# Kernel optimization log

Measured on AMD Instinct MI355X. Metric: run time of the kernel, lower is better.

## Reference

```python
import jax, jax.numpy as jnp
import numpy as np

N = 32       # number of variables (per-var LSTMs)
L = 128      # window length
D = 128      # hidden dim
HEADS = 8
TAU_MAX = 5
ALPHA = 0.7  # attn_decay_alpha
B = 128      # number of time-ordered windows


def setup_inputs() -> dict:
    key = jax.random.key(0)
    ks = jax.random.split(key, 20)
    s = 0.1
    f = lambda k, shape: (jax.random.normal(k, shape, jnp.float32) * s)
    return {
        "X": jax.random.normal(ks[0], (B, L, N), jnp.float32),
        # per-variable encoder LSTM (input size 1): W_ih (N,4D), W_hh (N,4D,D), combined-style biases kept separate
        "enc_Wih": f(ks[1], (N, 4 * D)),
        "enc_Whh": f(ks[2], (N, 4 * D, D)),
        "enc_b": f(ks[3], (N, 4 * D)),            # b_ih + b_hh merged (mathematically identical)
        "pool_w": f(ks[4], (N, D)),
        "pool_b": f(ks[5], (N,)),
        # shared MultiheadAttention params (torch layout: in_proj (3D,D))
        "in_proj_w": f(ks[6], (3 * D, D)),
        "in_proj_b": f(ks[7], (3 * D,)),
        "out_proj_w": f(ks[8], (D, D)),
        "out_proj_b": f(ks[9], (D,)),
        # per-variable decoder: init_h/init_c Linear(d,d), LSTM(1,d) (input is all-zeros so W_ih drops out), out Linear(d,1)
        "dec_initH_w": f(ks[10], (N, D, D)),
        "dec_initH_b": f(ks[11], (N, D)),
        "dec_initC_w": f(ks[12], (N, D, D)),
        "dec_initC_b": f(ks[13], (N, D)),
        "dec_Whh": f(ks[14], (N, 4 * D, D)),
        "dec_bih": f(ks[15], (N, 4 * D)),
        "dec_bhh": f(ks[16], (N, 4 * D)),
        "dec_out_w": f(ks[17], (N, D)),
        "dec_out_b": f(ks[18], (N,)),
    }


def _lstm_cell(gates, c):
    # torch gate order: i, f, g, o
    i, fg, g, o = jnp.split(gates, 4, axis=-1)
    i = jax.nn.sigmoid(i); fg = jax.nn.sigmoid(fg)
    g = jnp.tanh(g); o = jax.nn.sigmoid(o)
    c = fg * c + i * g
    h = o * jnp.tanh(c)
    return h, c


def _encode(X, Wih, Whh, b, pool_w, pool_b):
    # X: (B,L,N); encoder consumes first L-1 steps of each variable, batched over all N vars
    x = jnp.transpose(X[:, :-1, :], (1, 2, 0))  # (T, N, B)
    Bn = X.shape[0]
    h0 = jnp.zeros((N, Bn, D), X.dtype)

    def step(carry, x_t):  # x_t: (N,B)
        h, c = carry
        gates = (x_t[..., None] * Wih[:, None, :]
                 + jnp.einsum('nbd,ngd->nbg', h, Whh)
                 + b[:, None, :])
        h, c = _lstm_cell(gates, c)
        return (h, c), h

    _, H = jax.lax.scan(step, (h0, h0), x)  # H: (T,N,B,D)
    # TemporalAttnPool: softmax over time of a linear score, weighted sum
    scores = jnp.einsum('tnbd,nd->tnb', H, pool_w) + pool_b[None, :, None]
    a = jax.nn.softmax(scores, axis=0)
    C = jnp.einsum('tnb,tnbd->bnd', a, H)  # (B,N,D)
    return C


def _mha(Q, KV, in_w, in_b, out_w, out_b):
    dh = D // HEADS
    q = Q @ in_w[:D].T + in_b[:D]
    k = KV @ in_w[D:2 * D].T + in_b[D:2 * D]
    v = KV @ in_w[2 * D:].T + in_b[2 * D:]
    sp = lambda x: x.reshape(x.shape[0], x.shape[1], HEADS, dh)
    q, k, v = sp(q), sp(k), sp(v)
    scores = jnp.einsum('bqhd,bkhd->bhqk', q, k) / float(np.sqrt(dh))
    attn = jax.nn.softmax(scores, axis=-1)
    o = jnp.einsum('bhqk,bkhd->bqhd', attn, v).reshape(Q.shape)
    return o @ out_w.T + out_b


def _cross_attend(C, in_w, in_b, out_w, out_b):
    Bn = C.shape[0]
    tmax = min(TAU_MAX, Bn - 1)
    if tmax <= 0:
        return C
    out_sum = jnp.zeros_like(C)
    w_sum = jnp.zeros((Bn, 1, 1), C.dtype)
    for tau in range(1, tmax + 1):  # small fixed loop over lags
        o = _mha(C[tau:], C[:-tau], in_w, in_b, out_w, out_b)
        w = float(np.exp(-ALPHA * (tau - 1)))  # attn_agg == 'decay'
        out_sum = out_sum.at[tau:].add(o * w)
        w_sum = w_sum.at[tau:].add(w)
    out = out_sum / jnp.clip(w_sum, 1e-8)
    return C + out  # residual=True


def _decode(C_star, iHw, iHb, iCw, iCb, Whh, bih, bhh, ow, ob):
    # h0/c0 from tanh(Linear(c_star)); LSTM input is all-zeros so input term reduces to b_ih
    h0 = jnp.tanh(jnp.einsum('bnd,ned->nbe', C_star, iHw) + iHb[:, None, :])
    c0 = jnp.tanh(jnp.einsum('bnd,ned->nbe', C_star, iCw) + iCb[:, None, :])
    b = (bih + bhh)[:, None, :]  # (N,1,4D)

    def step(carry, _):
        h, c = carry
        gates = jnp.einsum('nbd,ngd->nbg', h, Whh) + b
        h, c = _lstm_cell(gates, c)
        o = jnp.einsum('nbd,nd->nb', h, ow) + ob[:, None]
        return (h, c), o

    _, O = jax.lax.scan(step, (h0, c0), None, length=L)  # (L,N,B)
    recon = jnp.transpose(O[:L - 1], (2, 0, 1))  # (B,L-1,N)
    pred = O[L - 1].T                            # (B,N)
    return recon, pred


def reference(X, enc_Wih, enc_Whh, enc_b, pool_w, pool_b,
              in_proj_w, in_proj_b, out_proj_w, out_proj_b,
              dec_initH_w, dec_initH_b, dec_initC_w, dec_initC_b,
              dec_Whh, dec_bih, dec_bhh, dec_out_w, dec_out_b):
    C = _encode(X, enc_Wih, enc_Whh, enc_b, pool_w, pool_b)
    C_star = _cross_attend(C, in_proj_w, in_proj_b, out_proj_w, out_proj_b)
    recon, pred = _decode(C_star, dec_initH_w, dec_initH_b, dec_initC_w, dec_initC_b,
                          dec_Whh, dec_bih, dec_bhh, dec_out_w, dec_out_b)
    return recon, pred, C_star
```

## Files before the change

kernel.cpp:

```cpp
#include <hip/hip_runtime.h>
#include <hip/hip_bf16.h>

typedef unsigned short ushort_t;
typedef unsigned int uint_t;

#define DD   128
#define G4   512
#define BT   16
#define NB   128
#define NV   32

#define OFF_WIH   0
#define OFF_EB    16384
#define OFF_PW    32768
#define OFF_PB    36864
#define OFF_INW   37120
#define OFF_INB   86272
#define OFF_OUTW  86784
#define OFF_OUTB  103168
#define OFF_IHB   103424
#define OFF_ICB   107520
#define OFF_DBIH  111616
#define OFF_DBHH  128000
#define OFF_DOW   144384
#define OFF_DOB   148480
#define P_TOTAL   148736
#define OFF_FLAGS (OFF_PB + 32)

typedef __attribute__((ext_vector_type(8))) short bf16x8;
typedef __attribute__((ext_vector_type(4))) float f32x4;

__device__ __forceinline__ float bf2f(ushort_t u) {
    union { uint_t i; float f; } x; x.i = ((uint_t)u) << 16; return x.f;
}
__device__ __forceinline__ ushort_t f2bf(float f) {
    __hip_bfloat16 h = __float2bfloat16(f);
    return *(ushort_t*)&h;
}
__device__ __forceinline__ uint_t f2u(float f) {
    union { float f; uint_t i; } x; x.f = f; return x.i;
}
__device__ __forceinline__ float u2f(uint_t u) {
    union { uint_t i; float f; } x; x.i = u; return x.f;
}
__device__ __forceinline__ float exp2_f(float x) {
    float r; asm("v_exp_f32 %0, %1" : "=v"(r) : "v"(x)); return r;
}
__device__ __forceinline__ float sigmoid_f(float x) {
    return __builtin_amdgcn_rcpf(1.f + exp2_f(x * -1.442695041f));
}
__device__ __forceinline__ float tanh_f(float x) {
    return 1.f - 2.f * __builtin_amdgcn_rcpf(exp2_f(x * 2.885390082f) + 1.f);
}
__device__ __forceinline__ uint_t cvt_pk_bf16(float a, float b) {
    uint_t r; asm("v_cvt_pk_bf16_f32 %0, %1, %2" : "=v"(r) : "v"(a), "v"(b)); return r;
}
__device__ __forceinline__ bf16x8 pack8(f32x4 a, f32x4 b) {
    union { uint_t u[4]; bf16x8 v; } x;
    x.u[0] = cvt_pk_bf16(a.x, a.y); x.u[1] = cvt_pk_bf16(a.z, a.w);
    x.u[2] = cvt_pk_bf16(b.x, b.y); x.u[3] = cvt_pk_bf16(b.z, b.w);
    return x.v;
}
__device__ __forceinline__ float swz_bcast_l15(float v) {
    return u2f((uint_t)__builtin_amdgcn_ds_swizzle((int)f2u(v), 0x000F));
}
__device__ __forceinline__ void store_out(void* out, long idx, float v, int bf) {
    if (bf) ((ushort_t*)out)[idx] = f2bf(v);
    else    ((float*)out)[idx]    = v;
}
#define LBAR() do { asm volatile("s_waitcnt lgkmcnt(0)" ::: "memory"); \
                    __builtin_amdgcn_s_barrier(); } while (0)

__device__ __forceinline__ int wave_probe(const void* p, int elems) {
    int cap = elems < 1024 ? elems : 1024;
    int lane = threadIdx.x & 63;
    const ushort_t* u = (const ushort_t*)p;
    int cnt = 0, tot = 0;
    for (int j = lane; j < cap; j += 64) {
        ushort_t x = u[j];
        float af = fabsf(bf2f(x));
        tot++;
        if (x == 0 || (af > 1e-7f && af < 100.f)) cnt++;
    }
    #pragma unroll
    for (int off = 32; off >= 1; off >>= 1) {
        cnt += __shfl_xor(cnt, off);
        tot += __shfl_xor(tot, off);
    }
    return (cnt * 10 >= tot * 9) ? 1 : 0;
}

struct Ptr19 { const void* p[19]; };

__global__ __launch_bounds__(256) void prep_kernel(Ptr19 a, float* __restrict__ P,
                                                   float* __restrict__ Xc) {
    __shared__ float tile[32][65];
    if (blockIdx.x < 581) {
        int base = blockIdx.x * 256;
        int src, o0, size;
        if      (base < OFF_EB)   { src = 1;  o0 = base - OFF_WIH;  size = 16384; }
        else if (base < OFF_PW)   { src = 3;  o0 = base - OFF_EB;   size = 16384; }
        else if (base < OFF_PB)   { src = 4;  o0 = base - OFF_PW;   size = 4096;  }
        else if (base < OFF_INW)  { src = 5;  o0 = base - OFF_PB;   size = 32;    }
        else if (base < OFF_INB)  { src = 6;  o0 = base - OFF_INW;  size = 49152; }
        else if (base < OFF_OUTW) { src = 7;  o0 = base - OFF_INB;  size = 384;   }
        else if (base < OFF_OUTB) { src = 8;  o0 = base - OFF_OUTW; size = 16384; }
        else if (base < OFF_IHB)  { src = 9;  o0 = base - OFF_OUTB; size = 128;   }
        else if (base < OFF_ICB)  { src = 11; o0 = base - OFF_IHB;  size = 4096;  }
        else if (base < OFF_DBIH) { src = 13; o0 = base - OFF_ICB;  size = 4096;  }
        else if (base < OFF_DBHH) { src = 15; o0 = base - OFF_DBIH; size = 16384; }
        else if (base < OFF_DOW)  { src = 16; o0 = base - OFF_DBHH; size = 16384; }
        else if (base < OFF_DOB)  { src = 17; o0 = base - OFF_DOW;  size = 4096;  }
        else                      { src = 18; o0 = base - OFF_DOB;  size = 32;    }
        int bf = wave_probe(a.p[src], size);
        int off = o0 + (int)threadIdx.x;
        if (off < size)
            P[base + threadIdx.x] = bf ? bf2f(((const ushort_t*)a.p[src])[off])
                                       : ((const float*)a.p[src])[off];
    } else if (blockIdx.x < 837) {
        int bf = wave_probe(a.p[0], 1024);
        int idx2 = blockIdx.x - 581;
        int bt = (idx2 & 3) * 32, tn0 = (idx2 >> 2) * 64;
        const void* src = a.p[0];
        int tx = threadIdx.x & 63, ty = threadIdx.x >> 6;
        #pragma unroll
        for (int k = 0; k < 8; k++) {
            int row = ty * 8 + k;
            int idx = (bt + row) * 4096 + tn0 + tx;
            tile[row][tx] = bf ? bf2f(((const ushort_t*)src)[idx]) : ((const float*)src)[idx];
        }
        __syncthreads();
        int bx = threadIdx.x & 31, tyy = threadIdx.x >> 5;
        #pragma unroll
        for (int k = 0; k < 8; k++) {
            int tn = tn0 + tyy * 8 + k;
            int t = tn >> 5, nn = tn & 31;
            Xc[t * 4096 + nn * 128 + bt + bx] = tile[bx][tyy * 8 + k];
        }
    } else {
        int which = blockIdx.x - 837;
        int src = (which == 0) ? 0 : (which == 1) ? 2 : (which == 2) ? 10
                : (which == 3) ? 12 : 14;
        int flag = wave_probe(a.p[src], 1024);
        if (threadIdx.x == 0) P[OFF_FLAGS + which] = (float)flag;
    }
}

__global__ __launch_bounds__(512, 2) void enc_kernel(
    const float* __restrict__ Xc, const void* __restrict__ Wraw,
    const float* __restrict__ P, float* __restrict__ Cout)
{
    const int n = blockIdx.y, b0 = blockIdx.x * BT;
    const int tid = threadIdx.x;
    const int w = tid >> 6, lane = tid & 63;
    const int l15 = lane & 15, quad = lane >> 4;
    const int wbf = P[OFF_FLAGS + 1] > 0.5f;
    const int bown = b0 + l15;

    __shared__ alignas(16) ushort_t hS[2][16 * 136];
    for (int i = tid; i < 16 * 136; i += 512) hS[0][i] = 0;

    bf16x8 afrag[4][4];
    #pragma unroll
    for (int typ = 0; typ < 4; typ++) {
        const int g = typ * 128 + 16 * w + l15;
        #pragma unroll
        for (int kc = 0; kc < 4; kc++) {
            const int base = (n * G4 + g) * DD + 32 * kc + 8 * quad;
            if (wbf) {
                afrag[typ][kc] = *(const bf16x8*)((const ushort_t*)Wraw + base);
            } else {
                const float* fp = (const float*)Wraw + base;
                afrag[typ][kc] = pack8(*(const f32x4*)fp, *(const f32x4*)(fp + 4));
            }
        }
    }

    bf16x8 pfrag[4];
    #pragma unroll
    for (int kc = 0; kc < 4; kc++) {
        bf16x8 tmp;
        #pragma unroll
        for (int j = 0; j < 8; j++)
            tmp[j] = (l15 == 0 || l15 == 8)
                   ? (short)f2bf(P[OFF_PW + n * DD + 32 * kc + 8 * quad + j]) : (short)0;
        pfrag[kc] = tmp;
    }

    f32x4 bias4[4], wih4[4];
    #pragma unroll
    for (int typ = 0; typ < 4; typ++) {
        int base = n * G4 + typ * 128 + 16 * w + 4 * quad;
        bias4[typ] = *(const f32x4*)&P[OFF_EB + base];
        wih4[typ]  = *(const f32x4*)&P[OFF_WIH + base];
    }
    const float pb_r = P[OFF_PB + n];
    const f32x4 pb4 = {pb_r, pb_r, pb_r, pb_r};

    float cst[4] = {0.f, 0.f, 0.f, 0.f};
    f32x4 hpair[2];
    hpair[0] = f32x4{0.f, 0.f, 0.f, 0.f};
    hpair[1] = f32x4{0.f, 0.f, 0.f, 0.f};
    f32x4 Cacc   = {0.f, 0.f, 0.f, 0.f};
    float lR = 0.f, pend = 0.f;

    const float* xnext = Xc + n * 128 + bown;
    float xq = *xnext;
    xnext += 4096;

    if (w & 4) __builtin_amdgcn_s_setprio(1);

#define ENC_STEP(T, RB)                                                              \
    do {                                                                             \
        LBAR();                                                                      \
        bf16x8 bh[4];                                                                \
        _Pragma("unroll")                                                            \
        for (int kc = 0; kc < 4; kc++)                                               \
            bh[kc] = *(const bf16x8*)&hS[RB][l15 * 136 + 32 * kc + 8 * quad];        \
        if ((T) >= 2) {         \
            float e = __expf(pend);                                                  \
            lR += e;                                                                 \
            f32x4 ev = {e, e, e, e};                                                 \
            Cacc += ev * hpair[RB];                                                  \
        }                                                                            \
        f32x4 xv = {xq, xq, xq, xq};                                                 \
        f32x4 acc[4];                                                                \
        _Pragma("unroll")                                                            \
        for (int typ = 0; typ < 4; typ++)                                            \
            acc[typ] = __builtin_amdgcn_mfma_f32_16x16x32_bf16(                      \
                afrag[typ][0], bh[0], bias4[typ] + xv * wih4[typ], 0, 0, 0);         \
        f32x4 accP = __builtin_amdgcn_mfma_f32_16x16x32_bf16(pfrag[0], bh[0], pb4, 0, 0, 0); \
        xq = *xnext; xnext += 4096;    \
        _Pragma("unroll")                                                            \
        for (int kc = 1; kc < 4; kc++) {                                             \
            accP = __builtin_amdgcn_mfma_f32_16x16x32_bf16(pfrag[kc], bh[kc], accP, 0, 0, 0); \
            _Pragma("unroll")                                                        \
            for (int typ = 0; typ < 4; typ++)                                        \
                acc[typ] = __builtin_amdgcn_mfma_f32_16x16x32_bf16(afrag[typ][kc], bh[kc], acc[typ], 0, 0, 0); \
        }                                                                            \
        if ((T) >= 1) pend = swz_bcast_l15(accP[0]);   \
        float hh[4];                                                                 \
        _Pragma("unroll")                                                            \
        for (int r = 0; r < 4; r++) {                                                \
            float ii = sigmoid_f(acc[0][r]);                                         \
            float ff = sigmoid_f(acc[1][r]);                                         \
            float g2 = tanh_f(acc[2][r]);                                            \
            float oo = sigmoid_f(acc[3][r]);                                         \
            float cc = ff * cst[r] + ii * g2;                                        \
            cst[r] = cc;                                                             \
            hh[r] = oo * tanh_f(cc);                                                 \
        }                                                                            \
        hpair[RB].x = hh[0]; hpair[RB].y = hh[1];                                    \
        hpair[RB].z = hh[2]; hpair[RB].w = hh[3];                                    \
        uint2 hw;                                                                    \
        hw.x = cvt_pk_bf16(hh[0], hh[1]);                                            \
        hw.y = cvt_pk_bf16(hh[2], hh[3]);                                            \
        *(uint2*)&hS[(RB) ^ 1][l15 * 136 + 16 * w + 4 * quad] = hw;                  \
    } while (0)

    for (int tp = 0; tp < 63; tp++) {
        ENC_STEP(2 * tp, 0);
        ENC_STEP(2 * tp + 1, 1);
    }
    ENC_STEP(126, 0);
#undef ENC_STEP

    LBAR();
    {
        float e = __expf(pend);
        lR += e;
        f32x4 ev = {e, e, e, e};
        Cacc += ev * hpair[1];

        f32x4 accP = __builtin_amdgcn_mfma_f32_16x16x32_bf16(
            pfrag[0], *(const bf16x8*)&hS[1][l15 * 136 + 8 * quad], pb4, 0, 0, 0);
        #pragma unroll
        for (int kc = 1; kc < 4; kc++) {
            bf16x8 bh = *(const bf16x8*)&hS[1][l15 * 136 + 32 * kc + 8 * quad];
            accP = __builtin_amdgcn_mfma_f32_16x16x32_bf16(pfrag[kc], bh, accP, 0, 0, 0);
        }
        float e2 = __expf(swz_bcast_l15(accP[0]));
        lR += e2;
        f32x4 ev2 = {e2, e2, e2, e2};
        Cacc += ev2 * hpair[0];
    }
    float inv = 1.f / lR;
    f32x4 iv = {inv, inv, inv, inv};
    f32x4 cv = Cacc * iv;
    *(f32x4*)&Cout[bown * (NV * DD) + n * DD + 16 * w + 4 * quad] = cv;
}

__global__ __launch_bounds__(256) void qkv_kernel(
    const float* __restrict__ C, const float* __restrict__ P,
    float* __restrict__ q, float* __restrict__ k, float* __restrict__ v)
{
    int b = blockIdx.x, p = blockIdx.y, tid = threadIdx.x;
    int j = tid & 127, half = tid >> 7;
    __shared__ float Cb[NV * DD];
    for (int i = tid; i < NV * DD; i += 256) Cb[i] = C[b * (NV * DD) + i];
    __syncthreads();

    const float* wrow = P + OFF_INW + (p * DD + j) * DD;
    float bias = P[OFF_INB + p * DD + j];
    float acc[16];
    #pragma unroll
    for (int nn = 0; nn < 16; nn++) acc[nn] = bias;

    for (int dc = 0; dc < DD; dc += 8) {
        float4 w0 = *(const float4*)&wrow[dc];
        float4 w1 = *(const float4*)&wrow[dc + 4];
        #pragma unroll
        for (int nn = 0; nn < 16; nn++) {
            const float* cb = &Cb[(half * 16 + nn) * DD + dc];
            float4 c0 = *(float4*)&cb[0];
            float4 c1 = *(float4*)&cb[4];
            acc[nn] += c0.x * w0.x + c0.y * w0.y + c0.z * w0.z + c0.w * w0.w
                     + c1.x * w1.x + c1.y * w1.y + c1.z * w1.z + c1.w * w1.w;
        }
    }
    float* dst = (p == 0) ? q : (p == 1) ? k : v;
    for (int nn = 0; nn < 16; nn++)
        dst[b * (NV * DD) + (half * 16 + nn) * DD + j] = acc[nn];
}

__global__ __launch_bounds__(128) void attn_kernel(
    const float* __restrict__ q, const float* __restrict__ k, const float* __restrict__ v,
    const float* __restrict__ C, const float* __restrict__ P,
    float* __restrict__ Cstar, void* __restrict__ dout)
{
    int b = blockIdx.x, half = blockIdx.y, tid = threadIdx.x;
    int obf = P[OFF_FLAGS + 0] > 0.5f;
    int n0 = half * 16;
    __shared__ float Qs[16 * DD], Ks[NV * DD], Vs[NV * DD];
    float* Os = Ks;
    for (int i = tid; i < 16 * DD; i += 128) Qs[i] = q[b * (NV * DD) + n0 * DD + i];
    __syncthreads();

    int hh = tid >> 4, qi = tid & 15;
    float qreg[16];
    #pragma unroll
    for (int u = 0; u < 4; u++) {
        float4 t4 = *(float4*)&Qs[qi * DD + hh * 16 + 4 * u];
        qreg[4*u] = t4.x; qreg[4*u+1] = t4.y; qreg[4*u+2] = t4.z; qreg[4*u+3] = t4.w;
    }

    float Oacc[16];
    #pragma unroll
    for (int u = 0; u < 16; u++) Oacc[u] = 0.f;
    float wsum = 0.f;
    int tmax = (b < 5) ? b : 5;

    float4 kr[8], vr[8];
#define ATT_LOAD(TAU)                                                            \
    do {                                                                         \
        const float4* kp = (const float4*)&k[(b - (TAU)) * (NV * DD)];           \
        const float4* vp = (const float4*)&v[(b - (TAU)) * (NV * DD)];           \
        _Pragma("unroll")                                                        \
        for (int u = 0; u < 8; u++) {                                            \
            kr[u] = kp[tid + 128 * u];                                           \
            vr[u] = vp[tid + 128 * u];                                           \
        }                                                                        \
    } while (0)

    if (tmax >= 1) ATT_LOAD(1);

    for (int tau = 1; tau <= tmax; tau++) {
        __syncthreads();
        #pragma unroll
        for (int u = 0; u < 8; u++) {
            ((float4*)Ks)[tid + 128 * u] = kr[u];
            ((float4*)Vs)[tid + 128 * u] = vr[u];
        }
        __syncthreads();
        if (tau < tmax) ATT_LOAD(tau + 1);

        float s[NV];
        #pragma unroll
        for (int kk = 0; kk < NV; kk++) {
            float a = 0.f;
            #pragma unroll
            for (int u = 0; u < 4; u++) {
                float4 kv = *(float4*)&Ks[kk * DD + hh * 16 + 4 * u];
                a += qreg[4*u] * kv.x + qreg[4*u+1] * kv.y
                   + qreg[4*u+2] * kv.z + qreg[4*u+3] * kv.w;
            }
            s[kk] = a * 0.25f;
        }
        float mm = s[0];
        #pragma unroll
        for (int kk = 1; kk < NV; kk++) mm = fmaxf(mm, s[kk]);
        float ssum = 0.f;
        #pragma unroll
        for (int kk = 0; kk < NV; kk++) { s[kk] = __expf(s[kk] - mm); ssum += s[kk]; }
        float wdk = __expf(-0.7f * (float)(tau - 1));
        wsum += wdk;
        float wr = wdk / ssum;
        #pragma unroll
        for (int u = 0; u < 4; u++) {
            float ax = 0.f, ay = 0.f, az = 0.f, aw = 0.f;
            #pragma unroll
            for (int kk = 0; kk < NV; kk++) {
                float4 vv = *(float4*)&Vs[kk * DD + hh * 16 + 4 * u];
                ax += s[kk] * vv.x; ay += s[kk] * vv.y;
                az += s[kk] * vv.z; aw += s[kk] * vv.w;
            }
            Oacc[4*u] += wr * ax; Oacc[4*u+1] += wr * ay;
            Oacc[4*u+2] += wr * az; Oacc[4*u+3] += wr * aw;
        }
    }
#undef ATT_LOAD

    __syncthreads();
    float winv = (b > 0) ? 1.f / wsum : 0.f;
    #pragma unroll
    for (int u = 0; u < 16; u++)
        Os[qi * DD + hh * 16 + u] = Oacc[u] * winv;
    __syncthreads();

    int j = tid;
    const float* wrow = P + OFF_OUTW + j * DD;
    float obias = P[OFF_OUTB + j];
    for (int nn = 0; nn < 16; nn++) {
        float a = (b > 0) ? obias : 0.f;
        for (int dc = 0; dc < DD; dc += 8) {
            float4 w0 = *(const float4*)&wrow[dc];
            float4 w1 = *(const float4*)&wrow[dc + 4];
            float4 o0 = *(float4*)&Os[nn * DD + dc];
            float4 o1 = *(float4*)&Os[nn * DD + dc + 4];
            a += o0.x*w0.x + o0.y*w0.y + o0.z*w0.z + o0.w*w0.w
               + o1.x*w1.x + o1.y*w1.y + o1.z*w1.z + o1.w*w1.w;
        }
        int nng = n0 + nn;
        float cs = C[b * (NV * DD) + nng * DD + j] + a;
        Cstar[b * (NV * DD) + nng * DD + j] = cs;
        store_out(dout, 524288 + b * (NV * DD) + nng * DD + j, cs, obf);
    }
}

__global__ __launch_bounds__(512, 2) void dec_kernel(
    const float* __restrict__ Cstar,
    const void* __restrict__ iHw, const void* __restrict__ iCw,
    const void* __restrict__ Wraw,
    const float* __restrict__ P, void* __restrict__ out)
{
    const int n = blockIdx.y, b0 = blockIdx.x * BT;
    const int tid = threadIdx.x;
    const int w = tid >> 6, lane = tid & 63;
    const int l15 = lane & 15, quad = lane >> 4;
    const int obf = P[OFF_FLAGS + 0] > 0.5f;
    const int hbf = P[OFF_FLAGS + 2] > 0.5f;
    const int cbf = P[OFF_FLAGS + 3] > 0.5f;
    const int wbf = P[OFF_FLAGS + 4] > 0.5f;
    const int bown = b0 + l15;

    __shared__ alignas(16) ushort_t hS[2][16 * 136];

    bf16x8 cstB[4];
    #pragma unroll
    for (int kc = 0; kc < 4; kc++) {
        const float* cp = &Cstar[bown * (NV * DD) + n * DD + 32 * kc + 8 * quad];
        cstB[kc] = pack8(*(const f32x4*)&cp[0], *(const f32x4*)&cp[4]);
    }
    float cst[4];
    {
        f32x4 hAcc = *(const f32x4*)&P[OFF_IHB + n * DD + 16 * w + 4 * quad];
        f32x4 cAcc = *(const f32x4*)&P[OFF_ICB + n * DD + 16 * w + 4 * quad];
        #pragma unroll
        for (int kc = 0; kc < 4; kc++) {
            const int base = (n * DD + 16 * w + l15) * DD + 32 * kc + 8 * quad;
            bf16x8 wA;
            if (hbf) wA = *(const bf16x8*)((const ushort_t*)iHw + base);
            else {
                const float* fp = (const float*)iHw + base;
                wA = pack8(*(const f32x4*)fp, *(const f32x4*)(fp + 4));
            }
            hAcc = __builtin_amdgcn_mfma_f32_16x16x32_bf16(wA, cstB[kc], hAcc, 0, 0, 0);
            if (cbf) wA = *(const bf16x8*)((const ushort_t*)iCw + base);
            else {
                const float* fp = (const float*)iCw + base;
                wA = pack8(*(const f32x4*)fp, *(const f32x4*)(fp + 4));
            }
            cAcc = __builtin_amdgcn_mfma_f32_16x16x32_bf16(wA, cstB[kc], cAcc, 0, 0, 0);
        }
        float h0 = tanh_f(hAcc[0]), h1 = tanh_f(hAcc[1]);
        float h2 = tanh_f(hAcc[2]), h3 = tanh_f(hAcc[3]);
        #pragma unroll
        for (int r = 0; r < 4; r++) cst[r] = tanh_f(cAcc[r]);
        uint2 hw;
        hw.x = cvt_pk_bf16(h0, h1);
        hw.y = cvt_pk_bf16(h2, h3);
        *(uint2*)&hS[0][l15 * 136 + 16 * w + 4 * quad] = hw;
    }

    bf16x8 afrag[4][4];
    #pragma unroll
    for (int typ = 0; typ < 4; typ++) {
        const int g = typ * 128 + 16 * w + l15;
        #pragma unroll
        for (int kc = 0; kc < 4; kc++) {
            const int base = (n * G4 + g) * DD + 32 * kc + 8 * quad;
            if (wbf) {
                afrag[typ][kc] = *(const bf16x8*)((const ushort_t*)Wraw + base);
            } else {
                const float* fp = (const float*)Wraw + base;
                afrag[typ][kc] = pack8(*(const f32x4*)fp, *(const f32x4*)(fp + 4));
            }
        }
    }

    bf16x8 pfrag[4];
    #pragma unroll
    for (int kc = 0; kc < 4; kc++) {
        bf16x8 tmp;
        #pragma unroll
        for (int j = 0; j < 8; j++)
            tmp[j] = (l15 == 0) ? (short)f2bf(P[OFF_DOW + n * DD + 32 * kc + 8 * quad + j]) : (short)0;
        pfrag[kc] = tmp;
    }

    f32x4 bias4[4];
    #pragma unroll
    for (int typ = 0; typ < 4; typ++) {
        int base = n * G4 + typ * 128 + 16 * w + 4 * quad;
        f32x4 b1 = *(const f32x4*)&P[OFF_DBIH + base];
        f32x4 b2 = *(const f32x4*)&P[OFF_DBHH + base];
        bias4[typ] = b1 + b2;
    }
    const float ob_r = P[OFF_DOB + n];
    const f32x4 ob4 = {ob_r, ob_r, ob_r, ob_r};

    if (w & 4) __builtin_amdgcn_s_setprio(1);

#define DEC_STEP(T, RB)                                                              \
    do {                                                                             \
        LBAR();                                                                      \
        bf16x8 bh[4];                                                                \
        _Pragma("unroll")                                                            \
        for (int kc = 0; kc < 4; kc++)                                               \
            bh[kc] = *(const bf16x8*)&hS[RB][l15 * 136 + 32 * kc + 8 * quad];        \
        f32x4 acc[4];                                                                \
        _Pragma("unroll")                                                            \
        for (int typ = 0; typ < 4; typ++)                                            \
            acc[typ] = __builtin_amdgcn_mfma_f32_16x16x32_bf16(afrag[typ][0], bh[0], bias4[typ], 0, 0, 0); \
        _Pragma("unroll")                                                            \
        for (int kc = 1; kc < 4; kc++)                                               \
            _Pragma("unroll")                                                        \
            for (int typ = 0; typ < 4; typ++)                                        \
                acc[typ] = __builtin_amdgcn_mfma_f32_16x16x32_bf16(afrag[typ][kc], bh[kc], acc[typ], 0, 0, 0); \
        if (w == ((T) & 7)) {    \
            f32x4 accP = __builtin_amdgcn_mfma_f32_16x16x32_bf16(pfrag[0], bh[0], ob4, 0, 0, 0); \
            _Pragma("unroll")                                                        \
            for (int kc = 1; kc < 4; kc++)                                           \
                accP = __builtin_amdgcn_mfma_f32_16x16x32_bf16(pfrag[kc], bh[kc], accP, 0, 0, 0); \
            if ((T) > 0 && quad == 0)                                                \
                store_out(out, (long)bown * 4064 + (long)((T) - 1) * NV + n, accP[0], obf); \
        }                                                                            \
        float hh[4];                                                                 \
        _Pragma("unroll")                                                            \
        for (int r = 0; r < 4; r++) {                                                \
            float ii = sigmoid_f(acc[0][r]);                                         \
            float ff = sigmoid_f(acc[1][r]);                                         \
            float g2 = tanh_f(acc[2][r]);                                            \
            float oo = sigmoid_f(acc[3][r]);                                         \
            float cc = ff * cst[r] + ii * g2;                                        \
            cst[r] = cc;                                                             \
            hh[r] = oo * tanh_f(cc);                                                 \
        }                                                                            \
        uint2 hw;                                                                    \
        hw.x = cvt_pk_bf16(hh[0], hh[1]);                                            \
        hw.y = cvt_pk_bf16(hh[2], hh[3]);                                            \
        *(uint2*)&hS[(RB) ^ 1][l15 * 136 + 16 * w + 4 * quad] = hw;                  \
    } while (0)

    for (int tp = 0; tp < 64; tp++) {
        DEC_STEP(2 * tp, 0);
        DEC_STEP(2 * tp + 1, 1);
    }
#undef DEC_STEP

    LBAR();
    if (w == 0) {
        f32x4 accP = __builtin_amdgcn_mfma_f32_16x16x32_bf16(
            pfrag[0], *(const bf16x8*)&hS[0][l15 * 136 + 8 * quad], ob4, 0, 0, 0);
        #pragma unroll
        for (int kc = 1; kc < 4; kc++) {
            bf16x8 bh = *(const bf16x8*)&hS[0][l15 * 136 + 32 * kc + 8 * quad];
            accP = __builtin_amdgcn_mfma_f32_16x16x32_bf16(pfrag[kc], bh, accP, 0, 0, 0);
        }
        if (quad == 0)
            store_out(out, 520192 + (long)bown * NV + n, accP[0], obf);
    }
}

extern "C" void kernel_launch(void* const* d_in, const int* in_sizes, int n_in,
                              void* d_out, int out_size, void* d_ws, size_t ws_size,
                              hipStream_t stream) {
    char* ws = (char*)d_ws;
    float*    P    = (float*)(ws + 0);
    float*    Xc   = (float*)(ws + (1u << 20));
    float*    C    = (float*)(ws + (3u << 20));
    float*    qb   = (float*)(ws + (5u << 20));
    float*    kb   = (float*)(ws + (7u << 20));
    float*    vb   = (float*)(ws + (9u << 20));
    float*    Cst  = (float*)(ws + (11u << 20));

    Ptr19 a;
    for (int i = 0; i < 19; i++) a.p[i] = d_in[i];

    prep_kernel<<<842, 256, 0, stream>>>(a, P, Xc);
    enc_kernel<<<dim3(8, 32), 512, 0, stream>>>(Xc, d_in[2], P, C);
    qkv_kernel<<<dim3(128, 3), 256, 0, stream>>>(C, P, qb, kb, vb);
    attn_kernel<<<dim3(128, 2), 128, 0, stream>>>(qb, kb, vb, C, P, Cst, d_out);
    dec_kernel<<<dim3(8, 32), 512, 0, stream>>>(Cst, d_in[10], d_in[12], d_in[14], P, d_out);
}
```

Before: 419.2 us.

## Split LSTM gate MFMAs into halves to overlap transcendentals; widen attention block

```diff
diff --git a/kernel.cpp b/kernel.cpp
--- a/kernel.cpp
+++ b/kernel.cpp
@@ -46,11 +46,13 @@
 __device__ __forceinline__ float exp2_f(float x) {
     float r; asm("v_exp_f32 %0, %1" : "=v"(r) : "v"(x)); return r;
 }
+#define L1C (-1.442695041f)
+#define L2C (2.885390082f)
 __device__ __forceinline__ float sigmoid_f(float x) {
-    return __builtin_amdgcn_rcpf(1.f + exp2_f(x * -1.442695041f));
+    return __builtin_amdgcn_rcpf(1.f + exp2_f(x * L1C));
 }
 __device__ __forceinline__ float tanh_f(float x) {
-    return 1.f - 2.f * __builtin_amdgcn_rcpf(exp2_f(x * 2.885390082f) + 1.f);
+    return 1.f - 2.f * __builtin_amdgcn_rcpf(exp2_f(x * L2C) + 1.f);
 }
 __device__ __forceinline__ uint_t cvt_pk_bf16(float a, float b) {
     uint_t r; asm("v_cvt_pk_bf16_f32 %0, %1, %2" : "=v"(r) : "v"(a), "v"(b)); return r;
@@ -224,28 +226,49 @@
             Cacc += ev * hpair[RB];                                                  \
         }                                                                            \
         f32x4 xv = {xq, xq, xq, xq};                                                 \
-        f32x4 acc[4];                                                                \
-        _Pragma("unroll")                                                            \
-        for (int typ = 0; typ < 4; typ++)                                            \
-            acc[typ] = __builtin_amdgcn_mfma_f32_16x16x32_bf16(                      \
-                afrag[typ][0], bh[0], bias4[typ] + xv * wih4[typ], 0, 0, 0);         \
-        f32x4 accP = __builtin_amdgcn_mfma_f32_16x16x32_bf16(pfrag[0], bh[0], pb4, 0, 0, 0); \
+             \
+        f32x4 a0 = __builtin_amdgcn_mfma_f32_16x16x32_bf16(                          \
+            afrag[0][0], bh[0], bias4[0] + xv * wih4[0], 0, 0, 0);                   \
+        f32x4 a1 = __builtin_amdgcn_mfma_f32_16x16x32_bf16(                          \
+            afrag[1][0], bh[0], bias4[1] + xv * wih4[1], 0, 0, 0);                   \
+        _Pragma("unroll")                                                            \
+        for (int kc = 1; kc < 4; kc++) {                                             \
+            a0 = __builtin_amdgcn_mfma_f32_16x16x32_bf16(afrag[0][kc], bh[kc], a0, 0, 0, 0); \
+            a1 = __builtin_amdgcn_mfma_f32_16x16x32_bf16(afrag[1][kc], bh[kc], a1, 0, 0, 0); \
+        }                                                                            \
+        float e_i[4], e_f[4];                                                        \
+        _Pragma("unroll")                                                            \
+        for (int r = 0; r < 4; r++) {                                                \
+            e_i[r] = exp2_f(a0[r] * L1C);                                            \
+            e_f[r] = exp2_f(a1[r] * L1C);                                            \
+        }                                                                            \
+                \
+        f32x4 a2 = __builtin_amdgcn_mfma_f32_16x16x32_bf16(                          \
+            afrag[2][0], bh[0], bias4[2] + xv * wih4[2], 0, 0, 0);                   \
+        f32x4 a3 = __builtin_amdgcn_mfma_f32_16x16x32_bf16(                          \
+            afrag[3][0], bh[0], bias4[3] + xv * wih4[3], 0, 0, 0);                   \
+        f32x4 aP = __builtin_amdgcn_mfma_f32_16x16x32_bf16(pfrag[0], bh[0], pb4, 0, 0, 0); \
         xq = *xnext; xnext += 4096;    \
         _Pragma("unroll")                                                            \
         for (int kc = 1; kc < 4; kc++) {                                             \
-            accP = __builtin_amdgcn_mfma_f32_16x16x32_bf16(pfrag[kc], bh[kc], accP, 0, 0, 0); \
-            _Pragma("unroll")                                                        \
-            for (int typ = 0; typ < 4; typ++)                                        \
-                acc[typ] = __builtin_amdgcn_mfma_f32_16x16x32_bf16(afrag[typ][kc], bh[kc], acc[typ], 0, 0, 0); \
-        }                                                                            \
-        if ((T) >= 1) pend = swz_bcast_l15(accP[0]);   \
+            a2 = __builtin_amdgcn_mfma_f32_16x16x32_bf16(afrag[2][kc], bh[kc], a2, 0, 0, 0); \
+            a3 = __builtin_amdgcn_mfma_f32_16x16x32_bf16(afrag[3][kc], bh[kc], a3, 0, 0, 0); \
+            aP = __builtin_amdgcn_mfma_f32_16x16x32_bf16(pfrag[kc], bh[kc], aP, 0, 0, 0); \
+        }                                                                            \
+        float e_g[4], e_o[4];                                                        \
+        _Pragma("unroll")                                                            \
+        for (int r = 0; r < 4; r++) {                                                \
+            e_g[r] = exp2_f(a2[r] * L2C);                                            \
+            e_o[r] = exp2_f(a3[r] * L1C);                                            \
+        }                                                                            \
+        if ((T) >= 1) pend = swz_bcast_l15(aP[0]);             \
         float hh[4];                                                                 \
         _Pragma("unroll")                                                            \
         for (int r = 0; r < 4; r++) {                                                \
-            float ii = sigmoid_f(acc[0][r]);                                         \
-            float ff = sigmoid_f(acc[1][r]);                                         \
-            float g2 = tanh_f(acc[2][r]);                                            \
-            float oo = sigmoid_f(acc[3][r]);                                         \
+            float ii = __builtin_amdgcn_rcpf(1.f + e_i[r]);                          \
+            float ff = __builtin_amdgcn_rcpf(1.f + e_f[r]);                          \
+            float g2 = 1.f - 2.f * __builtin_amdgcn_rcpf(e_g[r] + 1.f);              \
+            float oo = __builtin_amdgcn_rcpf(1.f + e_o[r]);                          \
             float cc = ff * cst[r] + ii * g2;                                        \
             cst[r] = cc;                                                             \
             hh[r] = oo * tanh_f(cc);                                                 \
@@ -323,7 +346,7 @@
         dst[b * (NV * DD) + (half * 16 + nn) * DD + j] = acc[nn];
 }
 
-__global__ __launch_bounds__(128) void attn_kernel(
+__global__ __launch_bounds__(256) void attn_kernel(
     const float* __restrict__ q, const float* __restrict__ k, const float* __restrict__ v,
     const float* __restrict__ C, const float* __restrict__ P,
     float* __restrict__ Cstar, void* __restrict__ dout)
@@ -333,10 +356,11 @@
     int n0 = half * 16;
     __shared__ float Qs[16 * DD], Ks[NV * DD], Vs[NV * DD];
     float* Os = Ks;
-    for (int i = tid; i < 16 * DD; i += 128) Qs[i] = q[b * (NV * DD) + n0 * DD + i];
+    for (int i = tid; i < 16 * DD; i += 256) Qs[i] = q[b * (NV * DD) + n0 * DD + i];
     __syncthreads();
 
-    int hh = tid >> 4, qi = tid & 15;
+    int qi = tid & 15, sub = (tid >> 4) & 1, hh = tid >> 5;
+    int kk0 = sub * 16;
     float qreg[16];
     #pragma unroll
     for (int u = 0; u < 4; u++) {
@@ -350,15 +374,15 @@
     float wsum = 0.f;
     int tmax = (b < 5) ? b : 5;
 
-    float4 kr[8], vr[8];
+    float4 kr[4], vr[4];
 #define ATT_LOAD(TAU)                                                            \
     do {                                                                         \
         const float4* kp = (const float4*)&k[(b - (TAU)) * (NV * DD)];           \
         const float4* vp = (const float4*)&v[(b - (TAU)) * (NV * DD)];           \
         _Pragma("unroll")                                                        \
-        for (int u = 0; u < 8; u++) {                                            \
-            kr[u] = kp[tid + 128 * u];                                           \
-            vr[u] = vp[tid + 128 * u];                                           \
+        for (int u = 0; u < 4; u++) {                                            \
+            kr[u] = kp[tid + 256 * u];                                           \
+            vr[u] = vp[tid + 256 * u];                                           \
         }                                                                        \
     } while (0)
 
@@ -367,20 +391,20 @@
     for (int tau = 1; tau <= tmax; tau++) {
         __syncthreads();
         #pragma unroll
-        for (int u = 0; u < 8; u++) {
-            ((float4*)Ks)[tid + 128 * u] = kr[u];
-            ((float4*)Vs)[tid + 128 * u] = vr[u];
+        for (int u = 0; u < 4; u++) {
+            ((float4*)Ks)[tid + 256 * u] = kr[u];
+            ((float4*)Vs)[tid + 256 * u] = vr[u];
         }
         __syncthreads();
         if (tau < tmax) ATT_LOAD(tau + 1);
 
-        float s[NV];
-        #pragma unroll
-        for (int kk = 0; kk < NV; kk++) {
+        float s[16];
+        #pragma unroll
+        for (int kk = 0; kk < 16; kk++) {
             float a = 0.f;
             #pragma unroll
             for (int u = 0; u < 4; u++) {
-                float4 kv = *(float4*)&Ks[kk * DD + hh * 16 + 4 * u];
+                float4 kv = *(float4*)&Ks[(kk0 + kk) * DD + hh * 16 + 4 * u];
                 a += qreg[4*u] * kv.x + qreg[4*u+1] * kv.y
                    + qreg[4*u+2] * kv.z + qreg[4*u+3] * kv.w;
             }
@@ -388,10 +412,12 @@
         }
         float mm = s[0];
         #pragma unroll
-        for (int kk = 1; kk < NV; kk++) mm = fmaxf(mm, s[kk]);
+        for (int kk = 1; kk < 16; kk++) mm = fmaxf(mm, s[kk]);
+        mm = fmaxf(mm, __shfl_xor(mm, 16));
         float ssum = 0.f;
         #pragma unroll
-        for (int kk = 0; kk < NV; kk++) { s[kk] = __expf(s[kk] - mm); ssum += s[kk]; }
+        for (int kk = 0; kk < 16; kk++) { s[kk] = __expf(s[kk] - mm); ssum += s[kk]; }
+        ssum += __shfl_xor(ssum, 16);
         float wdk = __expf(-0.7f * (float)(tau - 1));
         wsum += wdk;
         float wr = wdk / ssum;
@@ -399,8 +425,8 @@
         for (int u = 0; u < 4; u++) {
             float ax = 0.f, ay = 0.f, az = 0.f, aw = 0.f;
             #pragma unroll
-            for (int kk = 0; kk < NV; kk++) {
-                float4 vv = *(float4*)&Vs[kk * DD + hh * 16 + 4 * u];
+            for (int kk = 0; kk < 16; kk++) {
+                float4 vv = *(float4*)&Vs[(kk0 + kk) * DD + hh * 16 + 4 * u];
                 ax += s[kk] * vv.x; ay += s[kk] * vv.y;
                 az += s[kk] * vv.z; aw += s[kk] * vv.w;
             }
@@ -410,17 +436,23 @@
     }
 #undef ATT_LOAD
 
+    #pragma unroll
+    for (int u = 0; u < 16; u++) Oacc[u] += __shfl_xor(Oacc[u], 16);
+
     __syncthreads();
     float winv = (b > 0) ? 1.f / wsum : 0.f;
-    #pragma unroll
-    for (int u = 0; u < 16; u++)
-        Os[qi * DD + hh * 16 + u] = Oacc[u] * winv;
+    if (sub == 0) {
+        #pragma unroll
+        for (int u = 0; u < 16; u++)
+            Os[qi * DD + hh * 16 + u] = Oacc[u] * winv;
+    }
     __syncthreads();
 
-    int j = tid;
+    int j = tid & 127;
+    int half2 = tid >> 7;
     const float* wrow = P + OFF_OUTW + j * DD;
     float obias = P[OFF_OUTB + j];
-    for (int nn = 0; nn < 16; nn++) {
+    for (int nn = half2 * 8; nn < half2 * 8 + 8; nn++) {
         float a = (b > 0) ? obias : 0.f;
         for (int dc = 0; dc < DD; dc += 8) {
             float4 w0 = *(const float4*)&wrow[dc];
@@ -538,15 +570,28 @@
         _Pragma("unroll")                                                            \
         for (int kc = 0; kc < 4; kc++)                                               \
             bh[kc] = *(const bf16x8*)&hS[RB][l15 * 136 + 32 * kc + 8 * quad];        \
-        f32x4 acc[4];                                                                \
-        _Pragma("unroll")                                                            \
-        for (int typ = 0; typ < 4; typ++)                                            \
-            acc[typ] = __builtin_amdgcn_mfma_f32_16x16x32_bf16(afrag[typ][0], bh[0], bias4[typ], 0, 0, 0); \
-        _Pragma("unroll")                                                            \
-        for (int kc = 1; kc < 4; kc++)                                               \
-            _Pragma("unroll")                                                        \
-            for (int typ = 0; typ < 4; typ++)                                        \
-                acc[typ] = __builtin_amdgcn_mfma_f32_16x16x32_bf16(afrag[typ][kc], bh[kc], acc[typ], 0, 0, 0); \
+                                                             \
+        f32x4 a0 = __builtin_amdgcn_mfma_f32_16x16x32_bf16(afrag[0][0], bh[0], bias4[0], 0, 0, 0); \
+        f32x4 a1 = __builtin_amdgcn_mfma_f32_16x16x32_bf16(afrag[1][0], bh[0], bias4[1], 0, 0, 0); \
+        _Pragma("unroll")                                                            \
+        for (int kc = 1; kc < 4; kc++) {                                             \
+            a0 = __builtin_amdgcn_mfma_f32_16x16x32_bf16(afrag[0][kc], bh[kc], a0, 0, 0, 0); \
+            a1 = __builtin_amdgcn_mfma_f32_16x16x32_bf16(afrag[1][kc], bh[kc], a1, 0, 0, 0); \
+        }                                                                            \
+        float e_i[4], e_f[4];                                                        \
+        _Pragma("unroll")                                                            \
+        for (int r = 0; r < 4; r++) {                                                \
+            e_i[r] = exp2_f(a0[r] * L1C);                                            \
+            e_f[r] = exp2_f(a1[r] * L1C);                                            \
+        }                                                                            \
+                                       \
+        f32x4 a2 = __builtin_amdgcn_mfma_f32_16x16x32_bf16(afrag[2][0], bh[0], bias4[2], 0, 0, 0); \
+        f32x4 a3 = __builtin_amdgcn_mfma_f32_16x16x32_bf16(afrag[3][0], bh[0], bias4[3], 0, 0, 0); \
+        _Pragma("unroll")                                                            \
+        for (int kc = 1; kc < 4; kc++) {                                             \
+            a2 = __builtin_amdgcn_mfma_f32_16x16x32_bf16(afrag[2][kc], bh[kc], a2, 0, 0, 0); \
+            a3 = __builtin_amdgcn_mfma_f32_16x16x32_bf16(afrag[3][kc], bh[kc], a3, 0, 0, 0); \
+        }                                                                            \
         if (w == ((T) & 7)) {    \
             f32x4 accP = __builtin_amdgcn_mfma_f32_16x16x32_bf16(pfrag[0], bh[0], ob4, 0, 0, 0); \
             _Pragma("unroll")                                                        \
@@ -555,13 +600,19 @@
             if ((T) > 0 && quad == 0)                                                \
                 store_out(out, (long)bown * 4064 + (long)((T) - 1) * NV + n, accP[0], obf); \
         }                                                                            \
+        float e_g[4], e_o[4];                                                        \
+        _Pragma("unroll")                                                            \
+        for (int r = 0; r < 4; r++) {                                                \
+            e_g[r] = exp2_f(a2[r] * L2C);                                            \
+            e_o[r] = exp2_f(a3[r] * L1C);                                            \
+        }                                                                            \
         float hh[4];                                                                 \
         _Pragma("unroll")                                                            \
         for (int r = 0; r < 4; r++) {                                                \
-            float ii = sigmoid_f(acc[0][r]);                                         \
-            float ff = sigmoid_f(acc[1][r]);                                         \
-            float g2 = tanh_f(acc[2][r]);                                            \
-            float oo = sigmoid_f(acc[3][r]);                                         \
+            float ii = __builtin_amdgcn_rcpf(1.f + e_i[r]);                          \
+            float ff = __builtin_amdgcn_rcpf(1.f + e_f[r]);                          \
+            float g2 = 1.f - 2.f * __builtin_amdgcn_rcpf(e_g[r] + 1.f);              \
+            float oo = __builtin_amdgcn_rcpf(1.f + e_o[r]);                          \
             float cc = ff * cst[r] + ii * g2;                                        \
             cst[r] = cc;                                                             \
             hh[r] = oo * tanh_f(cc);                                                 \
@@ -610,6 +661,6 @@
     prep_kernel<<<842, 256, 0, stream>>>(a, P, Xc);
     enc_kernel<<<dim3(8, 32), 512, 0, stream>>>(Xc, d_in[2], P, C);
     qkv_kernel<<<dim3(128, 3), 256, 0, stream>>>(C, P, qb, kb, vb);
-    attn_kernel<<<dim3(128, 2), 128, 0, stream>>>(qb, kb, vb, C, P, Cst, d_out);
+    attn_kernel<<<dim3(128, 2), 256, 0, stream>>>(qb, kb, vb, C, P, Cst, d_out);
     dec_kernel<<<dim3(8, 32), 512, 0, stream>>>(Cst, d_in[10], d_in[12], d_in[14], P, d_out);
 }
```

After: 412.7 us. Within noise of the previous version (-1.5%).
